# Performance work log

Measured on AMD Instinct MI355X. Metric: run time of the kernel, lower is better.

## Reference

```python
import jax, jax.numpy as jnp
import numpy as np

NUM_GROUPS = 64
TOPK = 8
BLOCK_M = 128
NUM_TOKENS = 8192
HIDDEN = 4096


def _build_perm(flat_ids_np, num_groups, block_m):
    """Single-pass histogram + stable sort + per-expert padding.

    Returns sorted_token_ids (int64, [total_padded]) and m_indices (int32,
    [total_padded]) exactly matching the torch per-expert loop semantics:
    each expert's slot list padded to a multiple of block_m by repeating its
    last slot (or zeros for empty experts).
    Output length is data-dependent, so this runs on host numpy (concrete
    values), mirroring the original module whose output shape is also
    data-dependent.
    """
    n = flat_ids_np.shape[0]
    order = np.argsort(flat_ids_np, kind="stable")  # token slots grouped by expert
    counts = np.bincount(flat_ids_np, minlength=num_groups)
    padded = (counts + block_m - 1) // block_m * block_m
    in_starts = np.concatenate([[0], np.cumsum(counts)])
    out_starts = np.concatenate([[0], np.cumsum(padded)])
    total = int(out_starts[-1])
    sorted_token_ids = np.zeros(total, dtype=np.int64)
    m_indices = np.zeros(total, dtype=np.int32)
    for e in range(num_groups):  # fixed small expert count
        c, p, o = int(counts[e]), int(padded[e]), int(out_starts[e])
        m_indices[o:o + p] = e
        if c > 0:
            seg = order[int(in_starts[e]):int(in_starts[e]) + c]
            sorted_token_ids[o:o + c] = seg
            sorted_token_ids[o + c:o + p] = seg[-1]  # pad with last slot
        # empty expert: rows stay zero (matches torch.zeros branch)
    np.clip(sorted_token_ids, None, n - 1, out=sorted_token_ids)
    return sorted_token_ids, m_indices


def setup_inputs() -> dict:
    key = jax.random.key(0)
    k1, k2 = jax.random.split(key)
    hidden_states = jax.random.normal(k1, (NUM_TOKENS, HIDDEN), dtype=jnp.bfloat16)
    topk_ids = jax.random.randint(k2, (NUM_TOKENS, TOPK), 0, NUM_GROUPS, dtype=jnp.int32)
    return {"hidden_states": hidden_states, "topk_ids": topk_ids}


def reference(hidden_states, topk_ids):
    m, _ = hidden_states.shape
    num_flat = m * TOPK
    flat_ids = np.asarray(topk_ids).reshape(-1)
    sorted_token_ids_np, m_indices_np = _build_perm(flat_ids, NUM_GROUPS, BLOCK_M)
    sorted_token_ids = jnp.asarray(sorted_token_ids_np)
    m_indices = jnp.asarray(m_indices_np)
    # inverse permutation for later unpermute (stable argsort breaks pad ties deterministically)
    inv_perm = jnp.argsort(sorted_token_ids, stable=True)[:num_flat]
    source_token_idx = sorted_token_ids // TOPK  # expert-contiguous gather indices
    output = hidden_states[source_token_idx]     # [total_padded, HIDDEN] bf16 gather
    return output, m_indices, inv_perm
```

## Files before the change

kernel.cpp:

```cpp
#include <hip/hip_runtime.h>
#include <hip/hip_bf16.h>

#define NG 64
#define TOPK 8
#define BM 128
#define NSLOT 65536
#define HID 4096
#define NTOK 8192
#define NSEG 64

typedef unsigned int v4u __attribute__((ext_vector_type(4)));


__global__ __launch_bounds__(256) void hist_scan_k(const int* __restrict__ ids,
                                                   int* __restrict__ ws) {
    __shared__ int h[NG], lm[NG];
    __shared__ int winner;
    int t = threadIdx.x, s = blockIdx.x;
    if (t < NG) { h[t] = 0; lm[t] = -1; }
    __syncthreads();
    int base = s * 1024;
    for (int i = t; i < 1024; i += 256) {
        int e = ids[base + i] & (NG - 1);
        atomicAdd(&h[e], 1);
        atomicMax(&lm[e], base + i);
    }
    __syncthreads();
    if (t < NG) {
        ws[320 + t * 64 + s] = h[t];
        ws[4416 + t * 64 + s] = lm[t];
    }
    __threadfence();
    __syncthreads();
    if (t == 0) {
        unsigned old = atomicAdd((unsigned*)&ws[257], 1u);
        winner = ((old & 63u) == 63u) ? 1 : 0;
    }
    __syncthreads();
    if (!winner) return;
    __threadfence();
    if (t < NG) {
        int e = t, c = 0, last = -1;
        for (int b = 0; b < NSEG; b++) {
            c += ws[320 + e * 64 + b];
            int l = ws[4416 + e * 64 + b];
            last = l > last ? l : last;
        }
        ws[64 + e] = c;
        ws[128 + e] = (c + BM - 1) / BM * BM;
        ws[192 + e] = last;
    }
    __syncthreads();
    if (t == 0) {
        int acc = 0;
        for (int f = 0; f < NG; f++) { ws[f] = acc; acc += ws[128 + f]; }
        ws[256] = acc;
    }
}

__global__ __launch_bounds__(64) void rank_k(const int* __restrict__ ids,
                                             const int* __restrict__ ws,
                                             unsigned short* __restrict__ rank) {
    int s = blockIdx.x;
    int lane = threadIdx.x;
    int base = 0;
    for (int s2 = 0; s2 < s; s2++) base += ws[320 + lane * 64 + s2];
    int segbase = s * 1024;
    unsigned long long below = (1ULL << lane) - 1ULL;
    for (int c0 = 0; c0 < 1024; c0 += 64) {
        int e = ids[segbase + c0 + lane] & (NG - 1);
        int r = 0;
#pragma unroll 8
        for (int x = 0; x < NG; x++) {
            unsigned long long m = __ballot(e == x);
            if (m) {
                int bx = __shfl(base, x);
                if (e == x) r = bx + __popcll(m & below);
                if (lane == x) base += (int)__popcll(m);
            }
        }
        rank[segbase + c0 + lane] = (unsigned short)r;
    }
}

__global__ __launch_bounds__(256) void copy_k(const __hip_bfloat16* __restrict__ hs,
                                              const int* __restrict__ ids,
                                              const int* __restrict__ ws,
                                              const unsigned short* __restrict__ rank,
                                              float* __restrict__ out) {
    __shared__ int s_last[NG], s_pad[NG];
    int b = blockIdx.x;
    int total = ws[256];
    int t = threadIdx.x;
    float* m_out = out + (size_t)total * HID;
    if (b < NTOK) {
        const v4u* s = (const v4u*)(hs + (size_t)b * HID);
        v4u w0 = s[t];
        v4u w1 = s[t + 256];
        v4u a0 = {w0.x << 16, w0.x & 0xFFFF0000u, w0.y << 16, w0.y & 0xFFFF0000u};
        v4u a1 = {w0.z << 16, w0.z & 0xFFFF0000u, w0.w << 16, w0.w & 0xFFFF0000u};
        v4u a2 = {w1.x << 16, w1.x & 0xFFFF0000u, w1.y << 16, w1.y & 0xFFFF0000u};
        v4u a3 = {w1.z << 16, w1.z & 0xFFFF0000u, w1.w << 16, w1.w & 0xFFFF0000u};
        int slot0 = b * TOPK;
#pragma unroll
        for (int k = 0; k < TOPK; k++) {
            int e = ids[slot0 + k] & (NG - 1);
            int dst = ws[e] + (int)rank[slot0 + k];
            if (dst < 0 || dst >= total) continue;
            v4u* d = (v4u*)(out + (size_t)dst * HID);
            d[2 * t] = a0;
            d[2 * t + 1] = a1;
            d[2 * (t + 256)] = a2;
            d[2 * (t + 256) + 1] = a3;
            if (t == 0) m_out[dst] = (float)e;
        }
    } else if (b < NTOK + NG * BM) {
        int q = b - NTOK;
        int e = q >> 7;
        int j = q & 127;
        int c = ws[64 + e], p = ws[128 + e];
        if (c + j >= p) return;
        int srcslot = ws[192 + e];
        int dst = ws[e] + c + j;
        if (dst < 0 || dst >= total) return;
        int src = srcslot >> 3;
        if (src < 0 || src >= NTOK) return;
        if (t == 0) m_out[dst] = (float)e;
        const v4u* s = (const v4u*)(hs + (size_t)src * HID);
        v4u* d = (v4u*)(out + (size_t)dst * HID);
#pragma unroll
        for (int half = 0; half < 2; half++) {
            int v = half * 256 + t;
            v4u w = s[v];
            v4u o1 = {w.x << 16, w.x & 0xFFFF0000u, w.y << 16, w.y & 0xFFFF0000u};
            v4u o2 = {w.z << 16, w.z & 0xFFFF0000u, w.w << 16, w.w & 0xFFFF0000u};
            d[2 * v] = o1;
            d[2 * v + 1] = o2;
        }
    } else {
        if (t < NG) {
            s_last[t] = ws[192 + t];
            s_pad[t] = ws[128 + t] - ws[64 + t];
        }
        __syncthreads();
        float* inv_out = out + (size_t)total * (HID + 1);
        int i = (b - NTOK - NG * BM) * 256 + t;
        int e = ids[i] & (NG - 1);
        int pos = ws[e] + (int)rank[i];
        int base = i;
#pragma unroll
        for (int f = 0; f < NG; f++) {
            int l = s_last[f];
            base += (l >= 0 && l < i) ? s_pad[f] : 0;
        }
        if (base < NSLOT) inv_out[base] = (float)pos;
        if (i == s_last[e]) {
            int oc = ws[e] + ws[64 + e];
            int pd = s_pad[e];
            for (int j = 0; j < pd; j++) {
                int idx = base + 1 + j;
                if (idx >= NSLOT) break;
                inv_out[idx] = (float)(oc + j);
            }
        }
    }
}

extern "C" void kernel_launch(void* const* d_in, const int* in_sizes, int n_in,
                              void* d_out, int out_size, void* d_ws, size_t ws_size,
                              hipStream_t stream) {
    const __hip_bfloat16* hs = (const __hip_bfloat16*)d_in[0];
    const int* ids = (const int*)d_in[1];
    float* out = (float*)d_out;

    int* ws = (int*)d_ws;
    unsigned short* rank = (unsigned short*)(ws + 8704);

    hipLaunchKernelGGL(hist_scan_k, dim3(NSEG), dim3(256), 0, stream, ids, ws);
    hipLaunchKernelGGL(rank_k, dim3(NSEG), dim3(64), 0, stream, ids, ws, rank);
    hipLaunchKernelGGL(copy_k, dim3(NTOK + NG * BM + NSLOT / 256), dim3(256), 0, stream,
                       hs, ids, ws, rank, out);
}
```

Measured before the change: 303.9 us.

## Switch copy from scatter-by-token to gather-by-output-row via source-row map

Builds an inverse map from each padded output row to its source slot, written during ranking and padding-fill. The copy kernel then launches one block per output row that reads its source token row and writes one contiguous destination row, instead of one block per token reading once and scattering to eight destinations. This trades reuse of each source read (now up to eight reads of the same row, mostly L2-served) for ordered, coalesced destination writes and a uniform grid. It adds a small scattered write of the map in rank_k and a serial padding-fill loop in the last hist block.

After: 329.8 us. 8.5% more time.

```diff
diff --git a/kernel.cpp b/kernel.cpp
--- a/kernel.cpp
+++ b/kernel.cpp
@@ -8,12 +8,14 @@
 #define HID 4096
 #define NTOK 8192
 #define NSEG 64
+#define MAXROWS 73664
 
 typedef unsigned int v4u __attribute__((ext_vector_type(4)));
 
 
 __global__ __launch_bounds__(256) void hist_scan_k(const int* __restrict__ ids,
-                                                   int* __restrict__ ws) {
+                                                   int* __restrict__ ws,
+                                                   unsigned short* __restrict__ srcrow) {
     __shared__ int h[NG], lm[NG];
     __shared__ int winner;
     int t = threadIdx.x, s = blockIdx.x;
@@ -56,11 +58,19 @@
         for (int f = 0; f < NG; f++) { ws[f] = acc; acc += ws[128 + f]; }
         ws[256] = acc;
     }
+    __syncthreads();
+    for (int e = 0; e < NG; e++) {
+        int c = ws[64 + e], p = ws[128 + e];
+        int o = ws[e];
+        unsigned short ls = (unsigned short)ws[192 + e];
+        for (int j = c + t; j < p; j += 256) srcrow[o + j] = ls;
+    }
 }
 
 __global__ __launch_bounds__(64) void rank_k(const int* __restrict__ ids,
                                              const int* __restrict__ ws,
-                                             unsigned short* __restrict__ rank) {
+                                             unsigned short* __restrict__ rank,
+                                             unsigned short* __restrict__ srcrow) {
     int s = blockIdx.x;
     int lane = threadIdx.x;
     int base = 0;
@@ -68,7 +78,8 @@
     int segbase = s * 1024;
     unsigned long long below = (1ULL << lane) - 1ULL;
     for (int c0 = 0; c0 < 1024; c0 += 64) {
-        int e = ids[segbase + c0 + lane] & (NG - 1);
+        int slot = segbase + c0 + lane;
+        int e = ids[slot] & (NG - 1);
         int r = 0;
 #pragma unroll 8
         for (int x = 0; x < NG; x++) {
@@ -79,7 +90,8 @@
                 if (lane == x) base += (int)__popcll(m);
             }
         }
-        rank[segbase + c0 + lane] = (unsigned short)r;
+        rank[slot] = (unsigned short)r;
+        srcrow[ws[e] + r] = (unsigned short)slot;
     }
 }
 
@@ -87,56 +99,29 @@
                                               const int* __restrict__ ids,
                                               const int* __restrict__ ws,
                                               const unsigned short* __restrict__ rank,
+                                              const unsigned short* __restrict__ srcrow,
                                               float* __restrict__ out) {
     __shared__ int s_last[NG], s_pad[NG];
     int b = blockIdx.x;
     int total = ws[256];
     int t = threadIdx.x;
-    float* m_out = out + (size_t)total * HID;
-    if (b < NTOK) {
-        const v4u* s = (const v4u*)(hs + (size_t)b * HID);
+    if (b < MAXROWS) {
+        if (b >= total) return;
+        int slot = (int)srcrow[b];
+        int src = slot >> 3;
+        if (t == 0) out[(size_t)total * HID + b] = (float)(ids[slot] & (NG - 1));
+        const v4u* s = (const v4u*)(hs + (size_t)src * HID);
         v4u w0 = s[t];
         v4u w1 = s[t + 256];
         v4u a0 = {w0.x << 16, w0.x & 0xFFFF0000u, w0.y << 16, w0.y & 0xFFFF0000u};
         v4u a1 = {w0.z << 16, w0.z & 0xFFFF0000u, w0.w << 16, w0.w & 0xFFFF0000u};
         v4u a2 = {w1.x << 16, w1.x & 0xFFFF0000u, w1.y << 16, w1.y & 0xFFFF0000u};
         v4u a3 = {w1.z << 16, w1.z & 0xFFFF0000u, w1.w << 16, w1.w & 0xFFFF0000u};
-        int slot0 = b * TOPK;
-#pragma unroll
-        for (int k = 0; k < TOPK; k++) {
-            int e = ids[slot0 + k] & (NG - 1);
-            int dst = ws[e] + (int)rank[slot0 + k];
-            if (dst < 0 || dst >= total) continue;
-            v4u* d = (v4u*)(out + (size_t)dst * HID);
-            d[2 * t] = a0;
-            d[2 * t + 1] = a1;
-            d[2 * (t + 256)] = a2;
-            d[2 * (t + 256) + 1] = a3;
-            if (t == 0) m_out[dst] = (float)e;
-        }
-    } else if (b < NTOK + NG * BM) {
-        int q = b - NTOK;
-        int e = q >> 7;
-        int j = q & 127;
-        int c = ws[64 + e], p = ws[128 + e];
-        if (c + j >= p) return;
-        int srcslot = ws[192 + e];
-        int dst = ws[e] + c + j;
-        if (dst < 0 || dst >= total) return;
-        int src = srcslot >> 3;
-        if (src < 0 || src >= NTOK) return;
-        if (t == 0) m_out[dst] = (float)e;
-        const v4u* s = (const v4u*)(hs + (size_t)src * HID);
-        v4u* d = (v4u*)(out + (size_t)dst * HID);
-#pragma unroll
-        for (int half = 0; half < 2; half++) {
-            int v = half * 256 + t;
-            v4u w = s[v];
-            v4u o1 = {w.x << 16, w.x & 0xFFFF0000u, w.y << 16, w.y & 0xFFFF0000u};
-            v4u o2 = {w.z << 16, w.z & 0xFFFF0000u, w.w << 16, w.w & 0xFFFF0000u};
-            d[2 * v] = o1;
-            d[2 * v + 1] = o2;
-        }
+        v4u* d = (v4u*)(out + (size_t)b * HID);
+        d[2 * t] = a0;
+        d[2 * t + 1] = a1;
+        d[2 * (t + 256)] = a2;
+        d[2 * (t + 256) + 1] = a3;
     } else {
         if (t < NG) {
             s_last[t] = ws[192 + t];
@@ -144,7 +129,7 @@
         }
         __syncthreads();
         float* inv_out = out + (size_t)total * (HID + 1);
-        int i = (b - NTOK - NG * BM) * 256 + t;
+        int i = (b - MAXROWS) * 256 + t;
         int e = ids[i] & (NG - 1);
         int pos = ws[e] + (int)rank[i];
         int base = i;
@@ -175,9 +160,10 @@
 
     int* ws = (int*)d_ws;
     unsigned short* rank = (unsigned short*)(ws + 8704);
+    unsigned short* srcrow = (unsigned short*)(ws + 41472);
 
-    hipLaunchKernelGGL(hist_scan_k, dim3(NSEG), dim3(256), 0, stream, ids, ws);
-    hipLaunchKernelGGL(rank_k, dim3(NSEG), dim3(64), 0, stream, ids, ws, rank);
-    hipLaunchKernelGGL(copy_k, dim3(NTOK + NG * BM + NSLOT / 256), dim3(256), 0, stream,
-                       hs, ids, ws, rank, out);
+    hipLaunchKernelGGL(hist_scan_k, dim3(NSEG), dim3(256), 0, stream, ids, ws, srcrow);
+    hipLaunchKernelGGL(rank_k, dim3(NSEG), dim3(64), 0, stream, ids, ws, rank, srcrow);
+    hipLaunchKernelGGL(copy_k, dim3(MAXROWS + NSLOT / 256), dim3(256), 0, stream,
+                       hs, ids, ws, rank, srcrow, out);
 }
```
